# Kernel optimization log

Hardware: AMD Instinct MI355X
Metric: run time of the kernel (lower is better)

The kernel has to match this reference:

```python
import jax, jax.numpy as jnp
import numpy as np

# Quantum layer math: each qubit starts in |0>, gets RX(x_i) then RY(theta_i),
#   <Z_i> = cos(x_i) * cos(theta_i)
# (RX rotates z->cos(x); RY then scales the z-component by cos(theta)).

def setup_inputs() -> dict:
    key = jax.random.key(0)
    k1, k2, k3, k4 = jax.random.split(key, 4)
    B, S, E, F = 32, 4096, 128, 512  # embed_dim == n_qubits == 128
    x = jax.random.normal(k1, (B, S, E), dtype=jnp.float32)
    theta = jax.random.normal(k2, (E,), dtype=jnp.float32)
    W1 = jax.random.normal(k3, (F, E), dtype=jnp.float32) * (1.0 / np.sqrt(E))
    W2 = jax.random.normal(k4, (E, F), dtype=jnp.float32) * (1.0 / np.sqrt(F))
    return {"x": x, "theta": theta, "W1": W1, "W2": W2}


def reference(x, theta, W1, W2):
    # Quantum expectation layer, fully vectorized over batch and sequence.
    q = jnp.cos(x) * jnp.cos(theta)  # [B, S, E]
    # Dropout is identity at inference. linear1 (no bias) -> relu -> linear2 (no bias).
    h = jax.nn.relu(jnp.einsum('bse,fe->bsf', q, W1))  # [B, S, F]
    out = jnp.einsum('bsf,ef->bse', h, W2)             # [B, S, E]
    return out
```

## Files before the change

### kernel.cpp

```cpp
#include <hip/hip_runtime.h>
#include <stdint.h>

typedef __attribute__((ext_vector_type(8))) short short8;
typedef __attribute__((ext_vector_type(4))) float floatx4;
typedef __attribute__((ext_vector_type(2))) unsigned int uintx2;
typedef unsigned short u16;
typedef unsigned int u32;

#define EDIM 128
#define FDIM 512
#define BM 64
#define FC 128
#define QSTR (EDIM + 8)
#define HSTR (FC + 8)

__device__ __forceinline__ u32 f2bf_rne(float f) {
    u32 u = __builtin_bit_cast(u32, f);
    return (u + 0x7fffu + ((u >> 16) & 1u)) >> 16;
}
__device__ __forceinline__ u32 pk2bf(float lo, float hi) {
    return f2bf_rne(lo) | (f2bf_rne(hi) << 16);
}

__global__ __launch_bounds__(256) void ffq_prep(const float* __restrict__ W1,
                                                const float* __restrict__ W2,
                                                u16* __restrict__ wb) {
    int i4 = blockIdx.x * 256 + threadIdx.x;
    const float4* src = (i4 < 16384)
        ? (reinterpret_cast<const float4*>(W1) + i4)
        : (reinterpret_cast<const float4*>(W2) + (i4 - 16384));
    float4 v = *src;
    uintx2 p;
    p.x = pk2bf(v.x, v.y);
    p.y = pk2bf(v.z, v.w);
    *(reinterpret_cast<uintx2*>(wb) + i4) = p;
}

__global__ __launch_bounds__(512, 6) void ffq_main(const float* __restrict__ x,
                                                   const float* __restrict__ theta,
                                                   const u16* __restrict__ wb,
                                                   float* __restrict__ out) {
    __shared__ u16 qs[BM * QSTR];
    __shared__ u16 hs[2][BM * HSTR];

    const int t = threadIdx.x;
    const int lane = t & 63;
    const int wv = t >> 6;
    const int l15 = lane & 15;
    const int quad = lane >> 4;

    {
        const float4* xin = reinterpret_cast<const float4*>(x) +
                            (size_t)blockIdx.x * (BM * EDIM / 4);
        const int et = (t & 31) * 4;
        float c0 = __cosf(theta[et + 0]);
        float c1 = __cosf(theta[et + 1]);
        float c2 = __cosf(theta[et + 2]);
        float c3 = __cosf(theta[et + 3]);
        #pragma unroll
        for (int r = 0; r < 4; ++r) {
            int i = t + 512 * r;
            int m = i >> 5;
            float4 v = xin[i];
            uintx2 p;
            p.x = pk2bf(__cosf(v.x) * c0, __cosf(v.y) * c1);
            p.y = pk2bf(__cosf(v.z) * c2, __cosf(v.w) * c3);
            *reinterpret_cast<uintx2*>(&qs[m * QSTR + et]) = p;
        }
    }
    __syncthreads();

    const u16* W1b = wb;
    const u16* W2b = wb + FDIM * EDIM;

    floatx4 acc2[4];
    #pragma unroll
    for (int mt = 0; mt < 4; ++mt) acc2[mt] = (floatx4){0.f, 0.f, 0.f, 0.f};

    #pragma unroll
    for (int c = 0; c < 4; ++c) {
        u16* hb = hs[c & 1];

        floatx4 acc1[4];
        #pragma unroll
        for (int mt = 0; mt < 4; ++mt) acc1[mt] = (floatx4){0.f, 0.f, 0.f, 0.f};

        const int f0 = c * FC + wv * 16;
        short8 a1[4];
        #pragma unroll
        for (int k = 0; k < 4; ++k)
            a1[k] = *reinterpret_cast<const short8*>(
                W1b + (size_t)(f0 + l15) * EDIM + k * 32 + quad * 8);

        #pragma unroll
        for (int k = 0; k < 4; ++k) {
            const int kq = k * 32 + quad * 8;
            #pragma unroll
            for (int mt = 0; mt < 4; ++mt) {
                short8 bq = *reinterpret_cast<const short8*>(
                    &qs[(mt * 16 + l15) * QSTR + kq]);
                acc1[mt] = __builtin_amdgcn_mfma_f32_16x16x32_bf16(a1[k], bq, acc1[mt], 0, 0, 0);
            }
        }

        const int fl = wv * 16 + quad * 4;
        #pragma unroll
        for (int mt = 0; mt < 4; ++mt) {
            floatx4 v = acc1[mt];
            uintx2 p;
            p.x = pk2bf(fmaxf(v[0], 0.f), fmaxf(v[1], 0.f));
            p.y = pk2bf(fmaxf(v[2], 0.f), fmaxf(v[3], 0.f));
            *reinterpret_cast<uintx2*>(&hb[(mt * 16 + l15) * HSTR + fl]) = p;
        }
        __syncthreads();

        #pragma unroll
        for (int k = 0; k < 4; ++k) {
            const int kq = k * 32 + quad * 8;
            short8 a = *reinterpret_cast<const short8*>(
                W2b + (size_t)(wv * 16 + l15) * FDIM + c * FC + kq);
            #pragma unroll
            for (int mt = 0; mt < 4; ++mt) {
                short8 bh = *reinterpret_cast<const short8*>(
                    &hb[(mt * 16 + l15) * HSTR + kq]);
                acc2[mt] = __builtin_amdgcn_mfma_f32_16x16x32_bf16(a, bh, acc2[mt], 0, 0, 0);
            }
        }
    }

    float* op = out + (size_t)blockIdx.x * BM * EDIM;
    const int col = wv * 16 + quad * 4;
    #pragma unroll
    for (int mt = 0; mt < 4; ++mt) {
        *reinterpret_cast<floatx4*>(op + (mt * 16 + l15) * EDIM + col) = acc2[mt];
    }
}

extern "C" void kernel_launch(void* const* d_in, const int* in_sizes, int n_in,
                              void* d_out, int out_size, void* d_ws, size_t ws_size,
                              hipStream_t stream) {
    const float* x     = (const float*)d_in[0];
    const float* theta = (const float*)d_in[1];
    const float* W1    = (const float*)d_in[2];
    const float* W2    = (const float*)d_in[3];
    u16* wb    = (u16*)d_ws;
    float* out = (float*)d_out;

    ffq_prep<<<128, 256, 0, stream>>>(W1, W2, wb);
    ffq_main<<<2048, 512, 0, stream>>>(x, theta, wb, out);
}
```

Baseline: 179.4 us.

## Switch both GEMMs to 32x32x16 bf16 MFMA with 2x4 wave tiling

Replaces the 16x16x32 MFMA tiles, where each wave covered 16 output features across all 64 rows, with 32x32x16 MFMA tiles. The eight waves now form a 2x4 grid (row half by 32-feature group) for both linear layers. Each wave issues fewer, larger MFMAs per chunk and reads less LDS data per FLOP. In exchange, each wave loads its own W1/W2 fragment per k-step, and the epilogue and output stores use the 32x32 accumulator layout.

```diff
diff --git a/kernel.cpp b/kernel.cpp
--- a/kernel.cpp
+++ b/kernel.cpp
@@ -3,6 +3,7 @@
 
 typedef __attribute__((ext_vector_type(8))) short short8;
 typedef __attribute__((ext_vector_type(4))) float floatx4;
+typedef __attribute__((ext_vector_type(16))) float floatx16;
 typedef __attribute__((ext_vector_type(2))) unsigned int uintx2;
 typedef unsigned short u16;
 typedef unsigned int u32;
@@ -46,8 +47,10 @@
     const int t = threadIdx.x;
     const int lane = t & 63;
     const int wv = t >> 6;
-    const int l15 = lane & 15;
-    const int quad = lane >> 4;
+    const int l31 = lane & 31;
+    const int h5 = lane >> 5;
+    const int mg = wv & 1;
+    const int gg = wv >> 1;
 
     {
         const float4* xin = reinterpret_cast<const float4*>(x) +
@@ -73,66 +76,58 @@
     const u16* W1b = wb;
     const u16* W2b = wb + FDIM * EDIM;
 
-    floatx4 acc2[4];
-    #pragma unroll
-    for (int mt = 0; mt < 4; ++mt) acc2[mt] = (floatx4){0.f, 0.f, 0.f, 0.f};
+    floatx16 acc2 = {0.f,0.f,0.f,0.f,0.f,0.f,0.f,0.f,
+                     0.f,0.f,0.f,0.f,0.f,0.f,0.f,0.f};
+
+    const u16* qp = &qs[(mg * 32 + l31) * QSTR + h5 * 8];
+    const u16* hp0 = &hs[0][(mg * 32 + l31) * HSTR + h5 * 8];
+    const u16* hp1 = &hs[1][(mg * 32 + l31) * HSTR + h5 * 8];
 
     #pragma unroll
     for (int c = 0; c < 4; ++c) {
         u16* hb = hs[c & 1];
 
-        floatx4 acc1[4];
+        floatx16 acc1 = {0.f,0.f,0.f,0.f,0.f,0.f,0.f,0.f,
+                         0.f,0.f,0.f,0.f,0.f,0.f,0.f,0.f};
+        const u16* w1p = W1b + (size_t)(c * FC + gg * 32 + l31) * EDIM + h5 * 8;
         #pragma unroll
-        for (int mt = 0; mt < 4; ++mt) acc1[mt] = (floatx4){0.f, 0.f, 0.f, 0.f};
-
-        const int f0 = c * FC + wv * 16;
-        short8 a1[4];
-        #pragma unroll
-        for (int k = 0; k < 4; ++k)
-            a1[k] = *reinterpret_cast<const short8*>(
-                W1b + (size_t)(f0 + l15) * EDIM + k * 32 + quad * 8);
-
-        #pragma unroll
-        for (int k = 0; k < 4; ++k) {
-            const int kq = k * 32 + quad * 8;
-            #pragma unroll
-            for (int mt = 0; mt < 4; ++mt) {
-                short8 bq = *reinterpret_cast<const short8*>(
-                    &qs[(mt * 16 + l15) * QSTR + kq]);
-                acc1[mt] = __builtin_amdgcn_mfma_f32_16x16x32_bf16(a1[k], bq, acc1[mt], 0, 0, 0);
-            }
+        for (int k = 0; k < 8; ++k) {
+            short8 a = *reinterpret_cast<const short8*>(w1p + k * 16);
+            short8 b = *reinterpret_cast<const short8*>(qp + k * 16);
+            acc1 = __builtin_amdgcn_mfma_f32_32x32x16_bf16(a, b, acc1, 0, 0, 0);
         }
 
-        const int fl = wv * 16 + quad * 4;
+        const int hrow = (mg * 32 + l31) * HSTR;
         #pragma unroll
-        for (int mt = 0; mt < 4; ++mt) {
-            floatx4 v = acc1[mt];
+        for (int rq = 0; rq < 4; ++rq) {
+            const int fl = gg * 32 + rq * 8 + h5 * 4;
             uintx2 p;
-            p.x = pk2bf(fmaxf(v[0], 0.f), fmaxf(v[1], 0.f));
-            p.y = pk2bf(fmaxf(v[2], 0.f), fmaxf(v[3], 0.f));
-            *reinterpret_cast<uintx2*>(&hb[(mt * 16 + l15) * HSTR + fl]) = p;
+            p.x = pk2bf(fmaxf(acc1[rq * 4 + 0], 0.f), fmaxf(acc1[rq * 4 + 1], 0.f));
+            p.y = pk2bf(fmaxf(acc1[rq * 4 + 2], 0.f), fmaxf(acc1[rq * 4 + 3], 0.f));
+            *reinterpret_cast<uintx2*>(&hb[hrow + fl]) = p;
         }
         __syncthreads();
 
+        const u16* w2p = W2b + (size_t)(gg * 32 + l31) * FDIM + c * FC + h5 * 8;
+        const u16* hp = (c & 1) ? hp1 : hp0;
         #pragma unroll
-        for (int k = 0; k < 4; ++k) {
-            const int kq = k * 32 + quad * 8;
-            short8 a = *reinterpret_cast<const short8*>(
-                W2b + (size_t)(wv * 16 + l15) * FDIM + c * FC + kq);
-            #pragma unroll
-            for (int mt = 0; mt < 4; ++mt) {
-                short8 bh = *reinterpret_cast<const short8*>(
-                    &hb[(mt * 16 + l15) * HSTR + kq]);
-                acc2[mt] = __builtin_amdgcn_mfma_f32_16x16x32_bf16(a, bh, acc2[mt], 0, 0, 0);
-            }
+        for (int k = 0; k < 8; ++k) {
+            short8 a = *reinterpret_cast<const short8*>(w2p + k * 16);
+            short8 b = *reinterpret_cast<const short8*>(hp + k * 16);
+            acc2 = __builtin_amdgcn_mfma_f32_32x32x16_bf16(a, b, acc2, 0, 0, 0);
         }
     }
 
-    float* op = out + (size_t)blockIdx.x * BM * EDIM;
-    const int col = wv * 16 + quad * 4;
+    float* op = out + (size_t)blockIdx.x * BM * EDIM +
+                (mg * 32 + l31) * EDIM + gg * 32 + h5 * 4;
     #pragma unroll
-    for (int mt = 0; mt < 4; ++mt) {
-        *reinterpret_cast<floatx4*>(op + (mt * 16 + l15) * EDIM + col) = acc2[mt];
+    for (int rq = 0; rq < 4; ++rq) {
+        floatx4 v;
+        v[0] = acc2[rq * 4 + 0];
+        v[1] = acc2[rq * 4 + 1];
+        v[2] = acc2[rq * 4 + 2];
+        v[3] = acc2[rq * 4 + 3];
+        *reinterpret_cast<floatx4*>(op + rq * 8) = v;
     }
 }
 
```

Result: slower. 225.7 us (+25.8%).
